# Kernel tuning notes

Measured on AMD Instinct MI355X. Metric: run time of the kernel, lower is better.

## Reference

```python
import jax, jax.numpy as jnp
import numpy as np

D_MODEL = 512
NHEAD = 8
DIM = D_MODEL // NHEAD
EPS_ATT = 1e-6
EPS_LN = 1e-5


def layer_norm(x, gamma, beta):
    mu = jnp.mean(x, axis=-1, keepdims=True)
    var = jnp.mean(jnp.square(x - mu), axis=-1, keepdims=True)
    return (x - mu) * jax.lax.rsqrt(var + EPS_LN) * gamma + beta


def setup_inputs() -> dict:
    key = jax.random.key(0)
    ks = jax.random.split(key, 12)
    B, L = 4, 4096
    s = 1.0 / np.sqrt(D_MODEL)
    inp = {
        "q": jax.random.normal(ks[0], (B, L, D_MODEL), jnp.float32),
        "k": jax.random.normal(ks[1], (B, L, D_MODEL), jnp.float32),
        "v": jax.random.normal(ks[2], (B, L, D_MODEL), jnp.float32),
        # weights stored [in, out] so application is x @ W (== torch Linear with W.T)
        "Wq": jax.random.normal(ks[3], (D_MODEL, D_MODEL), jnp.float32) * s,
        "Wk": jax.random.normal(ks[4], (D_MODEL, D_MODEL), jnp.float32) * s,
        "Wv": jax.random.normal(ks[5], (D_MODEL, D_MODEL), jnp.float32) * s,
        "Wm": jax.random.normal(ks[6], (D_MODEL, D_MODEL), jnp.float32) * s,
        "W1": jax.random.normal(ks[7], (D_MODEL, 4 * D_MODEL), jnp.float32) * s,
        "W2": jax.random.normal(ks[8], (4 * D_MODEL, D_MODEL), jnp.float32) * (0.5 * s),
        "g1": jnp.ones((D_MODEL,), jnp.float32),
        "b1": jnp.zeros((D_MODEL,), jnp.float32),
        "g2": jnp.ones((D_MODEL,), jnp.float32),
        "b2": jnp.zeros((D_MODEL,), jnp.float32),
    }
    return inp


def reference(q, k, v, Wq, Wk, Wv, Wm, W1, W2, g1, b1, g2, b2):
    B, L, _ = q.shape
    S = k.shape[1]
    # projections -> [B, L, H, D]
    Qp = (q @ Wq).reshape(B, L, NHEAD, DIM)
    Kp = (k @ Wk).reshape(B, S, NHEAD, DIM)
    Vp = (v @ Wv).reshape(B, S, NHEAD, DIM)
    # elu+1 feature map linear attention
    Q = jax.nn.elu(Qp) + 1.0
    K = jax.nn.elu(Kp) + 1.0
    Vn = Vp / S
    KV = jnp.einsum('nshd,nshv->nhdv', K, Vn)          # [B,H,D,D]
    Z = 1.0 / (jnp.einsum('nlhd,nhd->nlh', Q, K.sum(axis=1)) + EPS_ATT)
    msg = jnp.einsum('nlhd,nhdv,nlh->nlhv', Q, KV, Z) * S  # [B,L,H,D]
    # merge + residual + norm1
    msg = msg.reshape(B, L, D_MODEL) @ Wm
    msg = layer_norm(msg + q, g1, b1)
    # FFN; note original adds mlp output to q (not norm1 output)
    ffn = jax.nn.relu(msg @ W1) @ W2
    out = layer_norm(q + ffn, g2, b2)
    return out
```

## Files before the change

kernel.cpp:

```cpp
#include <hip/hip_runtime.h>

typedef unsigned short u16;
typedef unsigned int u32;

typedef __bf16 bf16x8 __attribute__((ext_vector_type(8)));
typedef float f32x4 __attribute__((ext_vector_type(4)));

#define EPI_BF16 0
#define EPI_ELU1 1
#define EPI_RELU 2
#define EPI_ADDRES_F32 3
#define EPI_PROJ3 4

__device__ __forceinline__ float bf2f(u16 x) {
    u32 u = ((u32)x) << 16;
    return __uint_as_float(u);
}
__device__ __forceinline__ u16 f2bf(float f) {
    u32 u = __float_as_uint(f);
    u32 r = (u + 0x7FFFu + ((u >> 16) & 1u)) >> 16;
    return (u16)r;
}

__device__ __forceinline__ void gload_lds16(const u16* g, u16* l) {
    __builtin_amdgcn_global_load_lds(
        (const __attribute__((address_space(1))) u32*)g,
        (__attribute__((address_space(3))) u32*)l, 16, 0, 0);
}

__global__ __launch_bounds__(256) void f2b_k(const float* __restrict__ in,
                                             u16* __restrict__ out, int n) {
    int i = (blockIdx.x * 256 + threadIdx.x) * 4;
    if (i >= n) return;
    float4 f = *(const float4*)(in + i);
    ushort4 o;
    o.x = f2bf(f.x); o.y = f2bf(f.y); o.z = f2bf(f.z); o.w = f2bf(f.w);
    *(ushort4*)(out + i) = o;
}

__global__ void transpose_k(const float* __restrict__ in, u16* __restrict__ out,
                            int R, int C) {
    int idx = blockIdx.x * 256 + threadIdx.x;
    if (idx >= R * C) return;
    int c = idx / R, r = idx % R;
    out[idx] = f2bf(in[(long)r * C + c]);
}

__global__ __launch_bounds__(256) void gemm_bt(
    const u16* __restrict__ A, const u16* __restrict__ Bt,
    void* __restrict__ C, const float* __restrict__ Res,
    int M, int N, int K, int epi)
{
    __shared__ __align__(16) u16 As[2][4096];
    __shared__ __align__(16) u16 Bs[2][4096];

    int t = threadIdx.x;

    int gx = gridDim.x;
    int nwg = gx * gridDim.y;
    int bid = blockIdx.y * gx + blockIdx.x;
    if ((nwg & 7) == 0) {
        int cpx = nwg >> 3;
        bid = (bid & 7) * cpx + (bid >> 3);
    }
    int m0 = (bid / gx) * 128, n0 = (bid % gx) * 128;

    int third = 0;
    if (epi == EPI_PROJ3) {
        third = n0 >> 9;
        A += (long)third * 8388608;
    }

    int wave = t >> 6, lane = t & 63;
    int wm = (wave >> 1) * 64, wn = (wave & 1) * 64;
    int lrow = lane & 15;
    int kx = ((lane >> 4) ^ (lrow >> 2)) * 8;

    f32x4 acc[4][4] = {};

    int srow = wave * 16 + (lane >> 2);
    int scol = ((lane & 3) ^ (lane >> 4)) * 8;
    const u16* pA0 = A + (long)(m0 + srow) * K + scol;
    const u16* pB0 = Bt + (long)(n0 + srow) * K + scol;
    const long s64 = (long)64 * K;

    int nt = K >> 5;
    int cur = 0;

    {
        u16* a = As[0] + wave * 512;
        u16* b = Bs[0] + wave * 512;
        gload_lds16(pA0, a);
        gload_lds16(pA0 + s64, a + 2048);
        gload_lds16(pB0, b);
        gload_lds16(pB0 + s64, b + 2048);
    }
    __builtin_amdgcn_s_waitcnt(0);
    __syncthreads();

    for (int kt = 0; kt < nt; ++kt) {
        if (kt + 1 < nt) {
            int k0 = (kt + 1) << 5;
            u16* a = As[cur ^ 1] + wave * 512;
            u16* b = Bs[cur ^ 1] + wave * 512;
            gload_lds16(pA0 + k0, a);
            gload_lds16(pA0 + s64 + k0, a + 2048);
            gload_lds16(pB0 + k0, b);
            gload_lds16(pB0 + s64 + k0, b + 2048);
        }

        const u16* As_c = As[cur];
        const u16* Bs_c = Bs[cur];
        bf16x8 af[4], bfr[4];
#pragma unroll
        for (int mi = 0; mi < 4; mi++)
            af[mi] = *(const bf16x8*)(As_c + (wm + mi * 16 + lrow) * 32 + kx);
#pragma unroll
        for (int ni = 0; ni < 4; ni++)
            bfr[ni] = *(const bf16x8*)(Bs_c + (wn + ni * 16 + lrow) * 32 + kx);
#pragma unroll
        for (int mi = 0; mi < 4; mi++)
#pragma unroll
            for (int ni = 0; ni < 4; ni++)
                acc[mi][ni] = __builtin_amdgcn_mfma_f32_16x16x32_bf16(
                    af[mi], bfr[ni], acc[mi][ni], 0, 0, 0);

        if (kt + 1 < nt) {
            __builtin_amdgcn_s_waitcnt(0);
            __syncthreads();
            cur ^= 1;
        }
    }

    int rq = (lane >> 4) * 4;
    int colb = n0 + wn + (lane & 15);
#pragma unroll
    for (int mi = 0; mi < 4; mi++) {
#pragma unroll
        for (int ni = 0; ni < 4; ni++) {
#pragma unroll
            for (int r = 0; r < 4; r++) {
                int row = m0 + wm + mi * 16 + rq + r;
                int col = colb + ni * 16;
                float v0 = acc[mi][ni][r];
                if (epi == EPI_PROJ3) {
                    u16* Cb = (u16*)C + (long)third * 8388608;
                    long idx = (long)row * 512 + (col - (third << 9));
                    float v = (third < 2)
                                  ? (v0 > 0.f ? v0 + 1.f : __expf(v0))
                                  : v0;
                    Cb[idx] = f2bf(v);
                } else {
                    long idx = (long)row * N + col;
                    if (epi == EPI_ELU1) {
                        float v = v0 > 0.f ? v0 + 1.f : __expf(v0);
                        ((u16*)C)[idx] = f2bf(v);
                    } else if (epi == EPI_RELU) {
                        ((u16*)C)[idx] = f2bf(v0 > 0.f ? v0 : 0.f);
                    } else if (epi == EPI_ADDRES_F32) {
                        ((float*)C)[idx] = v0 + Res[idx];
                    } else {
                        ((u16*)C)[idx] = f2bf(v0);
                    }
                }
            }
        }
    }
}

__global__ __launch_bounds__(256) void kv_part(
    const u16* __restrict__ Kf, const u16* __restrict__ Vf,
    float* __restrict__ Part, float* __restrict__ KsPart)
{
    __shared__ float sKf[64 * 68];
    __shared__ float sVf[64 * 68];
    int bh = blockIdx.x;
    int b = bh >> 3, h = bh & 7;
    int t = threadIdx.x;
    int d = t & 63, vg = t >> 6;

    float acc[16] = {};
    float ks = 0.f;

    for (int st = 0; st < 2; ++st) {
        int s0 = blockIdx.y * 128 + st * 64;
        {
            int row = t >> 2, c16 = (t & 3) * 16;
            long g = ((long)b * 4096 + s0 + row) * 512 + h * 64 + c16;
            uint4 kk0 = *(const uint4*)(Kf + g);
            uint4 kk1 = *(const uint4*)(Kf + g + 8);
            uint4 vv0 = *(const uint4*)(Vf + g);
            uint4 vv1 = *(const uint4*)(Vf + g + 8);
            float* dk = sKf + row * 68 + c16;
            float* dv = sVf + row * 68 + c16;
            u32 kw[8] = {kk0.x, kk0.y, kk0.z, kk0.w, kk1.x, kk1.y, kk1.z, kk1.w};
            u32 vw[8] = {vv0.x, vv0.y, vv0.z, vv0.w, vv1.x, vv1.y, vv1.z, vv1.w};
#pragma unroll
            for (int j = 0; j < 8; j++) {
                dk[2 * j]     = __uint_as_float(kw[j] << 16);
                dk[2 * j + 1] = __uint_as_float(kw[j] & 0xFFFF0000u);
                dv[2 * j]     = __uint_as_float(vw[j] << 16);
                dv[2 * j + 1] = __uint_as_float(vw[j] & 0xFFFF0000u);
            }
        }
        __syncthreads();

#pragma unroll 4
        for (int s = 0; s < 64; s++) {
            float kd = sKf[s * 68 + d];
            if (vg == 0) ks += kd;
            const float* vr = sVf + s * 68 + vg * 16;
            float4 v0 = *(const float4*)(vr);
            float4 v1 = *(const float4*)(vr + 4);
            float4 v2 = *(const float4*)(vr + 8);
            float4 v3 = *(const float4*)(vr + 12);
            acc[0]  += kd * v0.x; acc[1]  += kd * v0.y;
            acc[2]  += kd * v0.z; acc[3]  += kd * v0.w;
            acc[4]  += kd * v1.x; acc[5]  += kd * v1.y;
            acc[6]  += kd * v1.z; acc[7]  += kd * v1.w;
            acc[8]  += kd * v2.x; acc[9]  += kd * v2.y;
            acc[10] += kd * v2.z; acc[11] += kd * v2.w;
            acc[12] += kd * v3.x; acc[13] += kd * v3.y;
            acc[14] += kd * v3.z; acc[15] += kd * v3.w;
        }
        __syncthreads();
    }

    float* pp = Part + ((long)bh * 32 + blockIdx.y) * 4096 + d * 64 + vg * 16;
#pragma unroll
    for (int j = 0; j < 16; j++) pp[j] = acc[j];
    if (vg == 0) KsPart[((bh * 32) + blockIdx.y) * 64 + d] = ks;
}

__global__ __launch_bounds__(256) void kv_reduce(
    const float* __restrict__ Part, const float* __restrict__ KsPart,
    float* __restrict__ KV, float* __restrict__ Ksum)
{
    int i = blockIdx.x * 256 + threadIdx.x;
    if (i < 131072) {
        int bh = i >> 12, dv = i & 4095;
        const float* p = Part + (long)bh * 32 * 4096 + dv;
        float s = 0.f;
#pragma unroll 8
        for (int sp = 0; sp < 32; sp++) s += p[(long)sp * 4096];
        KV[i] = s;
    } else if (i < 133120) {
        int j = i - 131072;
        int bh = j >> 6, d = j & 63;
        const float* p = KsPart + bh * 32 * 64 + d;
        float s = 0.f;
#pragma unroll 8
        for (int sp = 0; sp < 32; sp++) s += p[sp * 64];
        Ksum[j] = s;
    }
}

__global__ __launch_bounds__(256) void msg_k(
    const u16* __restrict__ Q, const float* __restrict__ KV,
    const float* __restrict__ Ksum, u16* __restrict__ Msg)
{
    __shared__ float sKVt[64 * 68];
    __shared__ float sQ[64 * 68];
    __shared__ float sKs[64];
    __shared__ float sZ[64];

    int bh = blockIdx.x;
    int b = bh >> 3, h = bh & 7;
    int l0 = blockIdx.y * 64;
    int t = threadIdx.x, wave = t >> 6, lane = t & 63;

    {
        const float* src = KV + (long)bh * 4096 + t * 16;
        int d = t >> 2;
        int v0 = (t & 3) * 16;
        float4 a0 = *(const float4*)(src);
        float4 a1 = *(const float4*)(src + 4);
        float4 a2 = *(const float4*)(src + 8);
        float4 a3 = *(const float4*)(src + 12);
        float tmp[16] = {a0.x, a0.y, a0.z, a0.w, a1.x, a1.y, a1.z, a1.w,
                         a2.x, a2.y, a2.z, a2.w, a3.x, a3.y, a3.z, a3.w};
#pragma unroll
        for (int j = 0; j < 16; j++) sKVt[(v0 + j) * 68 + d] = tmp[j];
    }
    {
        int row = t >> 2, c = (t & 3) * 16;
        const u16* src = Q + ((long)b * 4096 + l0 + row) * 512 + h * 64 + c;
        uint4 q0 = *(const uint4*)(src);
        uint4 q1 = *(const uint4*)(src + 8);
        float* dq = sQ + row * 68 + c;
        u32 qw[8] = {q0.x, q0.y, q0.z, q0.w, q1.x, q1.y, q1.z, q1.w};
#pragma unroll
        for (int j = 0; j < 8; j++) {
            dq[2 * j]     = __uint_as_float(qw[j] << 16);
            dq[2 * j + 1] = __uint_as_float(qw[j] & 0xFFFF0000u);
        }
    }
    if (t < 64) sKs[t] = Ksum[bh * 64 + t];
    __syncthreads();

    float kv[64];
    {
        const float* kr = sKVt + lane * 68;
#pragma unroll
        for (int j = 0; j < 16; j++) {
            float4 x = *(const float4*)(kr + 4 * j);
            kv[4 * j]     = x.x; kv[4 * j + 1] = x.y;
            kv[4 * j + 2] = x.z; kv[4 * j + 3] = x.w;
        }
    }
    if (t < 64) {
        const float* qr = sQ + t * 68;
        float zp = 0.f;
#pragma unroll
        for (int d = 0; d < 64; d++) zp += qr[d] * sKs[d];
        sZ[t] = 1.f / (zp + 1e-6f);
    }
    __syncthreads();

    const long obase = ((long)b * 4096 + l0) * 512 + h * 64 + lane;
    int lbase = wave * 16;
#pragma unroll 4
    for (int i = 0; i < 16; i++) {
        int ll = lbase + i;
        const float* qr = sQ + ll * 68;
        float a0 = 0.f, a1 = 0.f, a2 = 0.f, a3 = 0.f;
#pragma unroll
        for (int db = 0; db < 16; db++) {
            float4 q4 = *(const float4*)(qr + 4 * db);
            a0 += q4.x * kv[4 * db];
            a1 += q4.y * kv[4 * db + 1];
            a2 += q4.z * kv[4 * db + 2];
            a3 += q4.w * kv[4 * db + 3];
        }
        float acc = (a0 + a1) + (a2 + a3);
        Msg[obase + (long)ll * 512] = f2bf(acc * sZ[ll]);
    }
}

__global__ __launch_bounds__(256) void ln_k(
    const float* __restrict__ X, const float* __restrict__ g,
    const float* __restrict__ bta, u16* __restrict__ OutB,
    float* __restrict__ OutF, int out_f32)
{
    int row = blockIdx.x;
    const float* x = X + (long)row * 512;
    int t = threadIdx.x;
    float x0 = x[t], x1 = x[t + 256];
    float s = x0 + x1, sq = x0 * x0 + x1 * x1;
#pragma unroll
    for (int off = 32; off > 0; off >>= 1) {
        s += __shfl_xor(s, off, 64);
        sq += __shfl_xor(sq, off, 64);
    }
    __shared__ float rs[4], rq[4];
    int wave = t >> 6, lane = t & 63;
    if (lane == 0) { rs[wave] = s; rq[wave] = sq; }
    __syncthreads();
    s = rs[0] + rs[1] + rs[2] + rs[3];
    sq = rq[0] + rq[1] + rq[2] + rq[3];
    float mu = s * (1.f / 512.f);
    float var = sq * (1.f / 512.f) - mu * mu;
    float rstd = rsqrtf(var + 1e-5f);
    float y0 = (x0 - mu) * rstd * g[t] + bta[t];
    float y1 = (x1 - mu) * rstd * g[t + 256] + bta[t + 256];
    if (out_f32) {
        OutF[(long)row * 512 + t] = y0;
        OutF[(long)row * 512 + t + 256] = y1;
    } else {
        OutB[(long)row * 512 + t] = f2bf(y0);
        OutB[(long)row * 512 + t + 256] = f2bf(y1);
    }
}

extern "C" void kernel_launch(void* const* d_in, const int* in_sizes, int n_in,
                              void* d_out, int out_size, void* d_ws, size_t ws_size,
                              hipStream_t stream) {
    const float* q  = (const float*)d_in[0];
    const float* k  = (const float*)d_in[1];
    const float* v  = (const float*)d_in[2];
    const float* Wq = (const float*)d_in[3];
    const float* Wk = (const float*)d_in[4];
    const float* Wv = (const float*)d_in[5];
    const float* Wm = (const float*)d_in[6];
    const float* W1 = (const float*)d_in[7];
    const float* W2 = (const float*)d_in[8];
    const float* g1 = (const float*)d_in[9];
    const float* b1 = (const float*)d_in[10];
    const float* g2 = (const float*)d_in[11];
    const float* b2 = (const float*)d_in[12];

    char* ws = (char*)d_ws;
    u16* WTq = (u16*)(ws + 0);
    u16* WTk = (u16*)(ws + 524288);
    u16* WTv = (u16*)(ws + 1048576);
    u16* WTm = (u16*)(ws + 1572864);
    u16* W1T = (u16*)(ws + 2097152);
    u16* W2T = (u16*)(ws + 4194304);
    u16* qc  = (u16*)(ws + 6291456);
    u16* kc  = (u16*)(ws + 23068672);
    u16* vc  = (u16*)(ws + 39845888);
    u16* Qb  = (u16*)(ws + 56623104);
    u16* Kb  = (u16*)(ws + 73400320);
    u16* Vb  = (u16*)(ws + 90177536);
    float* KVb = (float*)(ws + 106954752);
    float* KSb = (float*)(ws + 107479040);
    u16* Msg = (u16*)(ws + 107487232);
    float* Part = (float*)(ws + 23068672);
    float* KsPart = (float*)(ws + 6291456);
    float* xpre = (float*)(ws + 23068672);
    u16* x1  = qc;
    u16* Hid = (u16*)(ws + 56623104);

    f2b_k<<<dim3(8192), 256, 0, stream>>>(q, qc, 8388608);
    f2b_k<<<dim3(8192), 256, 0, stream>>>(k, kc, 8388608);
    f2b_k<<<dim3(8192), 256, 0, stream>>>(v, vc, 8388608);

    transpose_k<<<dim3(1024), 256, 0, stream>>>(Wq, WTq, 512, 512);
    transpose_k<<<dim3(1024), 256, 0, stream>>>(Wk, WTk, 512, 512);
    transpose_k<<<dim3(1024), 256, 0, stream>>>(Wv, WTv, 512, 512);
    transpose_k<<<dim3(1024), 256, 0, stream>>>(Wm, WTm, 512, 512);
    transpose_k<<<dim3(4096), 256, 0, stream>>>(W1, W1T, 512, 2048);
    transpose_k<<<dim3(4096), 256, 0, stream>>>(W2, W2T, 2048, 512);

    gemm_bt<<<dim3(12, 128), 256, 0, stream>>>(qc, WTq, Qb, nullptr, 16384, 1536, 512, EPI_PROJ3);

    kv_part<<<dim3(32, 32), 256, 0, stream>>>(Kb, Vb, Part, KsPart);
    kv_reduce<<<dim3(520), 256, 0, stream>>>(Part, KsPart, KVb, KSb);
    msg_k<<<dim3(32, 64), 256, 0, stream>>>(Qb, KVb, KSb, Msg);

    gemm_bt<<<dim3(4, 128), 256, 0, stream>>>(Msg, WTm, xpre, q, 16384, 512, 512, EPI_ADDRES_F32);
    ln_k<<<dim3(16384), 256, 0, stream>>>(xpre, g1, b1, x1, nullptr, 0);

    gemm_bt<<<dim3(16, 128), 256, 0, stream>>>(x1, W1T, Hid, nullptr, 16384, 2048, 512, EPI_RELU);
    gemm_bt<<<dim3(4, 128), 256, 0, stream>>>(Hid, W2T, xpre, q, 16384, 512, 2048, EPI_ADDRES_F32);
    ln_k<<<dim3(16384), 256, 0, stream>>>(xpre, g2, b2, nullptr, (float*)d_out, 1);
}
```

Baseline: 509.6 us.

## Merge preprocessing launches, drop LDS swizzle, add K=64 GEMM for N=512 outputs

Folds the three fp32-to-bf16 conversions into one launch and the six weight transposes into two, which cuts launch overhead. Removes the XOR swizzle from the LDS load and read pattern in gemm_bt. Adds a gemm_bt64 variant that stages 64-wide K tiles so each barrier is followed by twice as much MFMA work, and uses it for the Wm and W2 GEMMs. Dropping the swizzle risks LDS bank conflicts on the fragment reads.

```diff
diff --git a/kernel.cpp b/kernel.cpp
--- a/kernel.cpp
+++ b/kernel.cpp
@@ -28,22 +28,42 @@
         (__attribute__((address_space(3))) u32*)l, 16, 0, 0);
 }
 
-__global__ __launch_bounds__(256) void f2b_k(const float* __restrict__ in,
-                                             u16* __restrict__ out, int n) {
-    int i = (blockIdx.x * 256 + threadIdx.x) * 4;
-    if (i >= n) return;
+__global__ __launch_bounds__(256) void f2b3_k(
+    const float* __restrict__ q, const float* __restrict__ k,
+    const float* __restrict__ v, u16* __restrict__ out) {
+    int bid = blockIdx.x;
+    int w = bid >> 13;
+    const float* in = (w == 0) ? q : (w == 1) ? k : v;
+    int i = ((bid & 8191) * 256 + threadIdx.x) * 4;
     float4 f = *(const float4*)(in + i);
     ushort4 o;
     o.x = f2bf(f.x); o.y = f2bf(f.y); o.z = f2bf(f.z); o.w = f2bf(f.w);
-    *(ushort4*)(out + i) = o;
-}
-
-__global__ void transpose_k(const float* __restrict__ in, u16* __restrict__ out,
-                            int R, int C) {
+    *(ushort4*)(out + (long)w * 8388608 + i) = o;
+}
+
+__global__ __launch_bounds__(256) void transpose4_k(
+    const float* __restrict__ W0, const float* __restrict__ W1,
+    const float* __restrict__ W2, const float* __restrict__ W3,
+    u16* __restrict__ out) {
     int idx = blockIdx.x * 256 + threadIdx.x;
-    if (idx >= R * C) return;
-    int c = idx / R, r = idx % R;
-    out[idx] = f2bf(in[(long)r * C + c]);
+    int w = idx >> 18, local = idx & 262143;
+    const float* in = (w == 0) ? W0 : (w == 1) ? W1 : (w == 2) ? W2 : W3;
+    int c = local >> 9, r = local & 511;
+    out[idx] = f2bf(in[r * 512 + c]);
+}
+
+__global__ __launch_bounds__(256) void transpose2_k(
+    const float* __restrict__ W1, const float* __restrict__ W2,
+    u16* __restrict__ out) {
+    int idx = blockIdx.x * 256 + threadIdx.x;
+    if (idx < 1048576) {
+        int c = idx / 512, r = idx % 512;
+        out[idx] = f2bf(W1[(long)r * 2048 + c]);
+    } else {
+        int local = idx - 1048576;
+        int c = local / 2048, r = local % 2048;
+        out[idx] = f2bf(W2[(long)r * 512 + c]);
+    }
 }
 
 __global__ __launch_bounds__(256) void gemm_bt(
@@ -55,7 +75,6 @@
     __shared__ __align__(16) u16 Bs[2][4096];
 
     int t = threadIdx.x;
-
     int gx = gridDim.x;
     int nwg = gx * gridDim.y;
     int bid = blockIdx.y * gx + blockIdx.x;
@@ -73,13 +92,12 @@
 
     int wave = t >> 6, lane = t & 63;
     int wm = (wave >> 1) * 64, wn = (wave & 1) * 64;
-    int lrow = lane & 15;
-    int kx = ((lane >> 4) ^ (lrow >> 2)) * 8;
+    int lrow = lane & 15, lk8 = (lane >> 4) * 8;
 
     f32x4 acc[4][4] = {};
 
     int srow = wave * 16 + (lane >> 2);
-    int scol = ((lane & 3) ^ (lane >> 4)) * 8;
+    int scol = (lane & 3) * 8;
     const u16* pA0 = A + (long)(m0 + srow) * K + scol;
     const u16* pB0 = Bt + (long)(n0 + srow) * K + scol;
     const long s64 = (long)64 * K;
@@ -114,10 +132,10 @@
         bf16x8 af[4], bfr[4];
 #pragma unroll
         for (int mi = 0; mi < 4; mi++)
-            af[mi] = *(const bf16x8*)(As_c + (wm + mi * 16 + lrow) * 32 + kx);
+            af[mi] = *(const bf16x8*)(As_c + (wm + mi * 16 + lrow) * 32 + lk8);
 #pragma unroll
         for (int ni = 0; ni < 4; ni++)
-            bfr[ni] = *(const bf16x8*)(Bs_c + (wn + ni * 16 + lrow) * 32 + kx);
+            bfr[ni] = *(const bf16x8*)(Bs_c + (wn + ni * 16 + lrow) * 32 + lk8);
 #pragma unroll
         for (int mi = 0; mi < 4; mi++)
 #pragma unroll
@@ -168,6 +186,120 @@
     }
 }
 
+__global__ __launch_bounds__(256) void gemm_bt64(
+    const u16* __restrict__ A, const u16* __restrict__ Bt,
+    void* __restrict__ C, const float* __restrict__ Res,
+    int M, int N, int K, int epi)
+{
+    __shared__ __align__(16) u16 As[2][8192];
+    __shared__ __align__(16) u16 Bs[2][8192];
+
+    int t = threadIdx.x;
+    int gx = gridDim.x;
+    int nwg = gx * gridDim.y;
+    int bid = blockIdx.y * gx + blockIdx.x;
+    if ((nwg & 7) == 0) {
+        int cpx = nwg >> 3;
+        bid = (bid & 7) * cpx + (bid >> 3);
+    }
+    int m0 = (bid / gx) * 128, n0 = (bid % gx) * 128;
+
+    int wave = t >> 6, lane = t & 63;
+    int wm = (wave >> 1) * 64, wn = (wave & 1) * 64;
+    int lrow = lane & 15, lk8 = (lane >> 4) * 8;
+
+    f32x4 acc[4][4] = {};
+
+    int srow = wave * 16 + (lane >> 2);
+    int scol = (lane & 3) * 8;
+    const u16* pA0 = A + (long)(m0 + srow) * K + scol;
+    const u16* pB0 = Bt + (long)(n0 + srow) * K + scol;
+    const long s64 = (long)64 * K;
+
+    int nt = K >> 6;
+    int cur = 0;
+
+    {
+        u16* a = As[0] + wave * 512;
+        u16* b = Bs[0] + wave * 512;
+#pragma unroll
+        for (int kk = 0; kk < 2; kk++) {
+            gload_lds16(pA0 + kk * 32, a + kk * 4096);
+            gload_lds16(pA0 + s64 + kk * 32, a + kk * 4096 + 2048);
+            gload_lds16(pB0 + kk * 32, b + kk * 4096);
+            gload_lds16(pB0 + s64 + kk * 32, b + kk * 4096 + 2048);
+        }
+    }
+    __builtin_amdgcn_s_waitcnt(0);
+    __syncthreads();
+
+    for (int kt = 0; kt < nt; ++kt) {
+        if (kt + 1 < nt) {
+            int k0 = (kt + 1) << 6;
+            u16* a = As[cur ^ 1] + wave * 512;
+            u16* b = Bs[cur ^ 1] + wave * 512;
+#pragma unroll
+            for (int kk = 0; kk < 2; kk++) {
+                gload_lds16(pA0 + k0 + kk * 32, a + kk * 4096);
+                gload_lds16(pA0 + s64 + k0 + kk * 32, a + kk * 4096 + 2048);
+                gload_lds16(pB0 + k0 + kk * 32, b + kk * 4096);
+                gload_lds16(pB0 + s64 + k0 + kk * 32, b + kk * 4096 + 2048);
+            }
+        }
+
+#pragma unroll
+        for (int kk = 0; kk < 2; kk++) {
+            const u16* As_c = As[cur] + kk * 4096;
+            const u16* Bs_c = Bs[cur] + kk * 4096;
+            bf16x8 af[4], bfr[4];
+#pragma unroll
+            for (int mi = 0; mi < 4; mi++)
+                af[mi] = *(const bf16x8*)(As_c + (wm + mi * 16 + lrow) * 32 + lk8);
+#pragma unroll
+            for (int ni = 0; ni < 4; ni++)
+                bfr[ni] = *(const bf16x8*)(Bs_c + (wn + ni * 16 + lrow) * 32 + lk8);
+#pragma unroll
+            for (int mi = 0; mi < 4; mi++)
+#pragma unroll
+                for (int ni = 0; ni < 4; ni++)
+                    acc[mi][ni] = __builtin_amdgcn_mfma_f32_16x16x32_bf16(
+                        af[mi], bfr[ni], acc[mi][ni], 0, 0, 0);
+        }
+
+        if (kt + 1 < nt) {
+            __builtin_amdgcn_s_waitcnt(0);
+            __syncthreads();
+            cur ^= 1;
+        }
+    }
+
+    int rq = (lane >> 4) * 4;
+    int colb = n0 + wn + (lane & 15);
+#pragma unroll
+    for (int mi = 0; mi < 4; mi++) {
+#pragma unroll
+        for (int ni = 0; ni < 4; ni++) {
+#pragma unroll
+            for (int r = 0; r < 4; r++) {
+                int row = m0 + wm + mi * 16 + rq + r;
+                int col = colb + ni * 16;
+                long idx = (long)row * N + col;
+                float v0 = acc[mi][ni][r];
+                if (epi == EPI_ELU1) {
+                    float v = v0 > 0.f ? v0 + 1.f : __expf(v0);
+                    ((u16*)C)[idx] = f2bf(v);
+                } else if (epi == EPI_RELU) {
+                    ((u16*)C)[idx] = f2bf(v0 > 0.f ? v0 : 0.f);
+                } else if (epi == EPI_ADDRES_F32) {
+                    ((float*)C)[idx] = v0 + Res[idx];
+                } else {
+                    ((u16*)C)[idx] = f2bf(v0);
+                }
+            }
+        }
+    }
+}
+
 __global__ __launch_bounds__(256) void kv_part(
     const u16* __restrict__ Kf, const u16* __restrict__ Vf,
     float* __restrict__ Part, float* __restrict__ KsPart)
@@ -391,14 +523,8 @@
 
     char* ws = (char*)d_ws;
     u16* WTq = (u16*)(ws + 0);
-    u16* WTk = (u16*)(ws + 524288);
-    u16* WTv = (u16*)(ws + 1048576);
-    u16* WTm = (u16*)(ws + 1572864);
     u16* W1T = (u16*)(ws + 2097152);
-    u16* W2T = (u16*)(ws + 4194304);
     u16* qc  = (u16*)(ws + 6291456);
-    u16* kc  = (u16*)(ws + 23068672);
-    u16* vc  = (u16*)(ws + 39845888);
     u16* Qb  = (u16*)(ws + 56623104);
     u16* Kb  = (u16*)(ws + 73400320);
     u16* Vb  = (u16*)(ws + 90177536);
@@ -411,16 +537,10 @@
     u16* x1  = qc;
     u16* Hid = (u16*)(ws + 56623104);
 
-    f2b_k<<<dim3(8192), 256, 0, stream>>>(q, qc, 8388608);
-    f2b_k<<<dim3(8192), 256, 0, stream>>>(k, kc, 8388608);
-    f2b_k<<<dim3(8192), 256, 0, stream>>>(v, vc, 8388608);
-
-    transpose_k<<<dim3(1024), 256, 0, stream>>>(Wq, WTq, 512, 512);
-    transpose_k<<<dim3(1024), 256, 0, stream>>>(Wk, WTk, 512, 512);
-    transpose_k<<<dim3(1024), 256, 0, stream>>>(Wv, WTv, 512, 512);
-    transpose_k<<<dim3(1024), 256, 0, stream>>>(Wm, WTm, 512, 512);
-    transpose_k<<<dim3(4096), 256, 0, stream>>>(W1, W1T, 512, 2048);
-    transpose_k<<<dim3(4096), 256, 0, stream>>>(W2, W2T, 2048, 512);
+    f2b3_k<<<dim3(24576), 256, 0, stream>>>(q, k, v, qc);
+
+    transpose4_k<<<dim3(4096), 256, 0, stream>>>(Wq, Wk, Wv, Wm, WTq);
+    transpose2_k<<<dim3(8192), 256, 0, stream>>>(W1, W2, W1T);
 
     gemm_bt<<<dim3(12, 128), 256, 0, stream>>>(qc, WTq, Qb, nullptr, 16384, 1536, 512, EPI_PROJ3);
 
@@ -428,10 +548,10 @@
     kv_reduce<<<dim3(520), 256, 0, stream>>>(Part, KsPart, KVb, KSb);
     msg_k<<<dim3(32, 64), 256, 0, stream>>>(Qb, KVb, KSb, Msg);
 
-    gemm_bt<<<dim3(4, 128), 256, 0, stream>>>(Msg, WTm, xpre, q, 16384, 512, 512, EPI_ADDRES_F32);
+    gemm_bt64<<<dim3(4, 128), 256, 0, stream>>>(Msg, (u16*)(ws + 1572864), xpre, q, 16384, 512, 512, EPI_ADDRES_F32);
     ln_k<<<dim3(16384), 256, 0, stream>>>(xpre, g1, b1, x1, nullptr, 0);
 
     gemm_bt<<<dim3(16, 128), 256, 0, stream>>>(x1, W1T, Hid, nullptr, 16384, 2048, 512, EPI_RELU);
-    gemm_bt<<<dim3(4, 128), 256, 0, stream>>>(Hid, W2T, xpre, q, 16384, 512, 2048, EPI_ADDRES_F32);
+    gemm_bt64<<<dim3(4, 128), 256, 0, stream>>>(Hid, (u16*)(ws + 4194304), xpre, q, 16384, 512, 2048, EPI_ADDRES_F32);
     ln_k<<<dim3(16384), 256, 0, stream>>>(xpre, g2, b2, nullptr, (float*)d_out, 1);
 }
```

Result: faster. 476.8 us (-6.4%).
